# Optimization experiments

Hardware: AMD Instinct MI355X
Metric: run time of the kernel (lower is better)

The kernel has to match this reference:

```python
import jax, jax.numpy as jnp
import numpy as np

B, N, D = 2, 2048, 1024
H = 16
D_HEAD = D // H
WINDOW = 128


def setup_inputs() -> dict:
    key = jax.random.key(0)
    ks = jax.random.split(key, 9)
    s = 1.0 / np.sqrt(D)
    return {
        "x": jax.random.normal(ks[0], (B, N, D), dtype=jnp.float32),
        "Wq": jax.random.uniform(ks[1], (D, D), jnp.float32, -s, s),
        "bq": jax.random.uniform(ks[2], (D,), jnp.float32, -s, s),
        "Wk": jax.random.uniform(ks[3], (D, D), jnp.float32, -s, s),
        "bk": jax.random.uniform(ks[4], (D,), jnp.float32, -s, s),
        "Wv": jax.random.uniform(ks[5], (D, D), jnp.float32, -s, s),
        "bv": jax.random.uniform(ks[6], (D,), jnp.float32, -s, s),
        "Wo": jax.random.uniform(ks[7], (D, D), jnp.float32, -s, s),
        "bo": jax.random.uniform(ks[8], (D,), jnp.float32, -s, s),
    }


def reference(x, Wq, bq, Wk, bk, Wv, bv, Wo, bo):
    # Projections (torch Linear: x @ W.T + b), split into heads: (B,H,N,d)
    def proj(W, b):
        y = x @ W.T + b
        return y.reshape(B, N, H, D_HEAD).transpose(0, 2, 1, 3)

    Q = proj(Wq, bq)
    K = proj(Wk, bk)
    V = proj(Wv, bv)

    scale = 1.0 / np.sqrt(D_HEAD)
    scores = jnp.einsum("bhqd,bhkd->bhqk", Q, K) * scale  # (B,H,N,N)

    i = jnp.arange(N)[:, None]
    j = jnp.arange(N)[None, :]
    band = jnp.abs(i - j) <= WINDOW  # (N,N) sliding-window band mask
    scores = jnp.where(band, scores, -jnp.inf)

    probs = jax.nn.softmax(scores, axis=-1)
    out = jnp.einsum("bhqk,bhkd->bhqd", probs, V)  # (B,H,N,d)
    out = out.transpose(0, 2, 1, 3).reshape(B, N, D)
    return out @ Wo.T + bo
```

## Files before the change

kernel.cpp:

```cpp
#include <hip/hip_runtime.h>
#include <hip/hip_bf16.h>
#include <stdint.h>

typedef __bf16 bf16_t;
typedef __bf16 bf16x8 __attribute__((ext_vector_type(8)));
typedef float f32x4 __attribute__((ext_vector_type(4)));

#define NB 2
#define NN 2048
#define ND 1024
#define NH 16
#define DHEAD 64
#define WIN 128

__device__ __forceinline__ void load_lds16(const void* g, void* l) {
  __builtin_amdgcn_global_load_lds(
      (const __attribute__((address_space(1))) uint32_t*)g,
      (__attribute__((address_space(3))) uint32_t*)l, 16, 0, 0);
}

__global__ __launch_bounds__(256) void cast_kernel(const float* __restrict__ in,
                                                   bf16_t* __restrict__ out, int n4) {
  int i = blockIdx.x * 256 + threadIdx.x;
  if (i < n4) {
    float4 v = reinterpret_cast<const float4*>(in)[i];
    union { bf16_t h[4]; uint2 u; } o;
    o.h[0] = (bf16_t)v.x; o.h[1] = (bf16_t)v.y;
    o.h[2] = (bf16_t)v.z; o.h[3] = (bf16_t)v.w;
    reinterpret_cast<uint2*>(out)[i] = o.u;
  }
}

__global__ __launch_bounds__(256) void cast4_kernel(const float* __restrict__ i0, const float* __restrict__ i1,
                                                    const float* __restrict__ i2, const float* __restrict__ i3,
                                                    bf16_t* o0, bf16_t* o1, bf16_t* o2, bf16_t* o3, int n4) {
  int z = blockIdx.y;
  const float* in = (z == 0) ? i0 : (z == 1) ? i1 : (z == 2) ? i2 : i3;
  bf16_t* out = (z == 0) ? o0 : (z == 1) ? o1 : (z == 2) ? o2 : o3;
  int i = blockIdx.x * 256 + threadIdx.x;
  if (i < n4) {
    float4 v = reinterpret_cast<const float4*>(in)[i];
    union { bf16_t h[4]; uint2 u; } o;
    o.h[0] = (bf16_t)v.x; o.h[1] = (bf16_t)v.y;
    o.h[2] = (bf16_t)v.z; o.h[3] = (bf16_t)v.w;
    reinterpret_cast<uint2*>(out)[i] = o.u;
  }
}

__global__ __launch_bounds__(512, 4)
void qkv_gemm8(const bf16_t* __restrict__ xb,
               const bf16_t* __restrict__ Wqb, const bf16_t* __restrict__ Wkb,
               const bf16_t* __restrict__ Wvb,
               const float* __restrict__ bq, const float* __restrict__ bk,
               const float* __restrict__ bv,
               bf16_t* __restrict__ Qh, bf16_t* __restrict__ Kh,
               bf16_t* __restrict__ VTt) {
  __shared__ __align__(16) bf16_t lds[3][12288];

  const int raw = blockIdx.x;
  const int swz = (raw & 7) * 48 + (raw >> 3);
  const int mt = swz / 12, nt = swz % 12;
  const int m0 = mt * 128;
  const int z = nt >> 2;
  const int n0z = (nt & 3) * 256;
  const bf16_t* Bw  = (z == 0) ? Wqb : (z == 1) ? Wkb : Wvb;
  const float* bias = (z == 0) ? bq  : (z == 1) ? bk  : bv;

  const int tid = threadIdx.x, lane = tid & 63, w = tid >> 6;
  const int wm = w >> 2, wn = w & 3;
  const int lrow = lane & 15, lkg = lane >> 4;
  const int srow = lane >> 2;
  const int schunk = (lane & 3) ^ (srow & 3);

  const bf16_t* asrc  = xb + (size_t)(m0 + w * 16 + srow) * 1024 + schunk * 8;
  const bf16_t* bsrc0 = Bw + (size_t)(n0z + (w * 2) * 16 + srow) * 1024 + schunk * 8;
  const bf16_t* bsrc1 = bsrc0 + 16 * 1024;

  f32x4 acc[4][4] = {};

  auto stage = [&](int t) {
    const int tt = (t < 32) ? t : (t - 32);
    const int k0 = tt << 5;
    bf16_t* buf = &lds[t % 3][0];
    load_lds16(asrc + k0,  buf + w * 512);
    load_lds16(bsrc0 + k0, buf + 4096 + (w * 2) * 512);
    load_lds16(bsrc1 + k0, buf + 4096 + (w * 2 + 1) * 512);
  };

  stage(0);
  stage(1);
  asm volatile("s_waitcnt vmcnt(3)" ::: "memory");
  __builtin_amdgcn_s_barrier();

  for (int t = 0; t < 32; ++t) {
    const bf16_t* Abuf = &lds[t % 3][0];
    const bf16_t* Bbuf = Abuf + 4096;
    bf16x8 af[4], bf[4];
#pragma unroll
    for (int m = 0; m < 4; ++m) {
      const int row = wm * 64 + m * 16 + lrow;
      af[m] = *reinterpret_cast<const bf16x8*>(Abuf + row * 32 + ((lkg ^ (row & 3)) << 3));
    }
#pragma unroll
    for (int n = 0; n < 4; ++n) {
      const int row = wn * 64 + n * 16 + lrow;
      bf[n] = *reinterpret_cast<const bf16x8*>(Bbuf + row * 32 + ((lkg ^ (row & 3)) << 3));
    }
    stage(t + 2);
    __builtin_amdgcn_s_barrier();
    __builtin_amdgcn_s_setprio(1);
#pragma unroll
    for (int m = 0; m < 4; ++m)
#pragma unroll
      for (int n = 0; n < 4; ++n)
        acc[m][n] = __builtin_amdgcn_mfma_f32_16x16x32_bf16(af[m], bf[n], acc[m][n], 0, 0, 0);
    __builtin_amdgcn_s_setprio(0);
    asm volatile("s_waitcnt vmcnt(3)" ::: "memory");
    __builtin_amdgcn_s_barrier();
    __builtin_amdgcn_sched_barrier(0);
  }

#pragma unroll
  for (int m = 0; m < 4; ++m)
#pragma unroll
    for (int n = 0; n < 4; ++n)
#pragma unroll
      for (int r = 0; r < 4; ++r) {
        const int grow = m0 + wm * 64 + m * 16 + lkg * 4 + r;
        const int colz = n0z + wn * 64 + n * 16 + lrow;
        float val = acc[m][n][r] + bias[colz];
        const int bb = grow >> 11, tok = grow & 2047;
        const int hh = colz >> 6, dd = colz & 63;
        if (z == 2) {
          VTt[((((size_t)(bb * NH + hh) * 32 + (tok >> 6)) * 64 + dd) << 6) + (tok & 63)] = (bf16_t)val;
        } else {
          bf16_t* outp = (z == 0) ? Qh : Kh;
          outp[(((size_t)(bb * NH + hh) * NN + tok) << 6) + dd] = (bf16_t)val;
        }
      }
}

__device__ __forceinline__ void gemm_tile(const bf16_t* __restrict__ A,
                                          const bf16_t* __restrict__ Bw,
                                          bf16_t* As, bf16_t* Bs,
                                          int m0, int n0, f32x4 acc[4][4]) {
  const int tid  = threadIdx.x;
  const int lane = tid & 63;
  const int wid  = tid >> 6;
  const int wr = wid >> 1, wc = wid & 1;
  const int lrow = lane & 15, lkg = lane >> 4;
  const int srow = lane >> 2, scol = (lane & 3) * 8;

  for (int k0 = 0; k0 < 1024; k0 += 32) {
#pragma unroll
    for (int i = 0; i < 2; ++i) {
      const int rbase = (wid * 2 + i) * 16;
      load_lds16(A  + (size_t)(m0 + rbase + srow) * 1024 + k0 + scol, As + rbase * 32);
      load_lds16(Bw + (size_t)(n0 + rbase + srow) * 1024 + k0 + scol, Bs + rbase * 32);
    }
    __syncthreads();
    bf16x8 af[4], bf[4];
#pragma unroll
    for (int m = 0; m < 4; ++m)
      af[m] = *reinterpret_cast<const bf16x8*>(As + (wr * 64 + m * 16 + lrow) * 32 + lkg * 8);
#pragma unroll
    for (int n = 0; n < 4; ++n)
      bf[n] = *reinterpret_cast<const bf16x8*>(Bs + (wc * 64 + n * 16 + lrow) * 32 + lkg * 8);
#pragma unroll
    for (int m = 0; m < 4; ++m)
#pragma unroll
      for (int n = 0; n < 4; ++n)
        acc[m][n] = __builtin_amdgcn_mfma_f32_16x16x32_bf16(af[m], bf[n], acc[m][n], 0, 0, 0);
    __syncthreads();
  }
}

__global__ __launch_bounds__(256, 2)
void out_gemm(const bf16_t* __restrict__ AOb, const bf16_t* __restrict__ Wob,
              const float* __restrict__ bo, float* __restrict__ Cout) {
  __shared__ __align__(16) bf16_t As[128 * 32];
  __shared__ __align__(16) bf16_t Bs[128 * 32];
  const int m0 = blockIdx.y * 128, n0 = blockIdx.x * 128;
  f32x4 acc[4][4] = {};
  gemm_tile(AOb, Wob, As, Bs, m0, n0, acc);

  const int lane = threadIdx.x & 63;
  const int wid  = threadIdx.x >> 6;
  const int wr = wid >> 1, wc = wid & 1;
  const int lrow = lane & 15, lkg = lane >> 4;
#pragma unroll
  for (int m = 0; m < 4; ++m)
#pragma unroll
    for (int n = 0; n < 4; ++n)
#pragma unroll
      for (int r = 0; r < 4; ++r) {
        int row = m0 + wr * 64 + m * 16 + lkg * 4 + r;
        int col = n0 + wc * 64 + n * 16 + lrow;
        Cout[(size_t)row * 1024 + col] = acc[m][n][r] + bo[col];
      }
}

__global__ __launch_bounds__(256)
void attn_kernel(const bf16_t* __restrict__ Qh, const bf16_t* __restrict__ Kh,
                 const bf16_t* __restrict__ VTt, bf16_t* __restrict__ AO) {
  __shared__ __align__(16) bf16_t KV_lds[2][2][4096];
  __shared__ uint32_t P_lds[4][16][32];

  const int work = ((blockIdx.x & 7) << 7) | (blockIdx.x >> 3);
  const int qt = work & 31, h = (work >> 5) & 15, b = work >> 9;
  const int tid = threadIdx.x, lane = tid & 63, w = tid >> 6;
  const int lrow = lane & 15, lkg = lane >> 4;
  const int q0 = qt * 64;
  const int qb = q0 + w * 16;
  const int qrow = qb + lrow;
  const int rs7 = lrow & 7;

  const int srow8 = lane >> 3;
  const int sswz  = 8 * ((lane & 7) ^ srow8);

  const bf16_t* kbase = Kh  + ((size_t)(b * NH + h) * NN) * DHEAD;
  const bf16_t* vbase = VTt + ((size_t)(b * NH + h) * (NN / 64)) * DHEAD * 64;

  const bf16_t* qptr = Qh + (((size_t)(b * NH + h) * NN + qrow) << 6) + lkg * 8;
  bf16x8 qf0 = *reinterpret_cast<const bf16x8*>(qptr);
  bf16x8 qf1 = *reinterpret_cast<const bf16x8*>(qptr + 32);

  float m_run = -1e30f, l_run = 0.f;
  f32x4 o[4] = {};

  const int kstart = (q0 - WIN > 0) ? (q0 - WIN) : 0;
  const int kend = (q0 + 64 + WIN < NN) ? (q0 + 64 + WIN) : NN;
  const int nch = (kend - kstart) >> 6;
  const float scale = 0.125f;

  auto stage = [&](int bufi, int kc) {
#pragma unroll
    for (int j = 0; j < 2; ++j) {
      const int i = w * 2 + j;
      load_lds16(kbase + (((size_t)(kc + i * 8 + srow8)) << 6) + sswz,
                 &KV_lds[bufi][0][i * 512]);
      load_lds16(vbase + (((size_t)((kc >> 6) * 64 + i * 8 + srow8)) << 6) + sswz,
                 &KV_lds[bufi][1][i * 512]);
    }
  };

  stage(0, kstart);
  __syncthreads();

  for (int ic = 0; ic < nch; ++ic) {
    const int kc = kstart + ic * 64;
    const int bi = ic & 1;
    if (ic + 1 < nch) stage(bi ^ 1, kc + 64);

    const bf16_t* Kt = &KV_lds[bi][0][0];
    const bf16_t* Vt = &KV_lds[bi][1][0];

    f32x4 s[4];
#pragma unroll
    for (int t = 0; t < 4; ++t) {
      const bf16_t* kr = Kt + (t * 16 + lrow) * 64;
      bf16x8 kf0 = *reinterpret_cast<const bf16x8*>(kr + ((lkg ^ rs7) << 3));
      bf16x8 kf1 = *reinterpret_cast<const bf16x8*>(kr + (((4 + lkg) ^ rs7) << 3));
      f32x4 zz = {};
      zz = __builtin_amdgcn_mfma_f32_16x16x32_bf16(kf0, qf0, zz, 0, 0, 0);
      zz = __builtin_amdgcn_mfma_f32_16x16x32_bf16(kf1, qf1, zz, 0, 0, 0);
      s[t] = zz;
    }

    bf16x8 vf0[4], vf1[4];
#pragma unroll
    for (int f = 0; f < 4; ++f) {
      const bf16_t* vr = Vt + (f * 16 + lrow) * 64;
      vf0[f] = *reinterpret_cast<const bf16x8*>(vr + ((lkg ^ rs7) << 3));
      vf1[f] = *reinterpret_cast<const bf16x8*>(vr + (((4 + lkg) ^ rs7) << 3));
    }

    const bool needs_mask = (kc < qb - 113) || (kc > qb + 65);
    float p[4][4];
    float mloc = -1e30f, rsum = 0.f;
    if (needs_mask) {
      float v[4][4];
#pragma unroll
      for (int t = 0; t < 4; ++t)
#pragma unroll
        for (int r = 0; r < 4; ++r) {
          int k = kc + t * 16 + lkg * 4 + r;
          int d = qrow - k;
          bool ok = (unsigned)(d + WIN) <= 2u * WIN;
          v[t][r] = ok ? s[t][r] * scale : -1e30f;
          mloc = fmaxf(mloc, v[t][r]);
        }
      mloc = fmaxf(mloc, __shfl_xor(mloc, 16, 64));
      mloc = fmaxf(mloc, __shfl_xor(mloc, 32, 64));
      float mn = fmaxf(m_run, mloc);
      float corr = __expf(m_run - mn);
      m_run = mn;
#pragma unroll
      for (int t = 0; t < 4; ++t)
#pragma unroll
        for (int r = 0; r < 4; ++r) {
          int k = kc + t * 16 + lkg * 4 + r;
          int d = qrow - k;
          bool ok = (unsigned)(d + WIN) <= 2u * WIN;
          p[t][r] = ok ? __expf(v[t][r] - mn) : 0.f;
          rsum += p[t][r];
        }
      rsum += __shfl_xor(rsum, 16, 64);
      rsum += __shfl_xor(rsum, 32, 64);
      l_run = l_run * corr + rsum;
#pragma unroll
      for (int f = 0; f < 4; ++f) o[f] *= corr;
    } else {
      float v[4][4];
#pragma unroll
      for (int t = 0; t < 4; ++t)
#pragma unroll
        for (int r = 0; r < 4; ++r) {
          v[t][r] = s[t][r] * scale;
          mloc = fmaxf(mloc, v[t][r]);
        }
      mloc = fmaxf(mloc, __shfl_xor(mloc, 16, 64));
      mloc = fmaxf(mloc, __shfl_xor(mloc, 32, 64));
      float mn = fmaxf(m_run, mloc);
      float corr = __expf(m_run - mn);
      m_run = mn;
#pragma unroll
      for (int t = 0; t < 4; ++t)
#pragma unroll
        for (int r = 0; r < 4; ++r) {
          p[t][r] = __expf(v[t][r] - mn);
          rsum += p[t][r];
        }
      rsum += __shfl_xor(rsum, 16, 64);
      rsum += __shfl_xor(rsum, 32, 64);
      l_run = l_run * corr + rsum;
#pragma unroll
      for (int f = 0; f < 4; ++f) o[f] *= corr;
    }

    uint32_t* prow = &P_lds[w][lrow][0];
#pragma unroll
    for (int t = 0; t < 4; ++t)
#pragma unroll
      for (int c = 0; c < 2; ++c) {
        union { bf16_t hh[2]; uint32_t u; } pk;
        pk.hh[0] = (bf16_t)p[t][2 * c];
        pk.hh[1] = (bf16_t)p[t][2 * c + 1];
        int L = 8 * t + 2 * lkg + c;
        int pos = (((L >> 2) ^ rs7) << 2) | (L & 3);
        prow[pos] = pk.u;
      }
    asm volatile("" ::: "memory");
    const bf16_t* prd = reinterpret_cast<const bf16_t*>(&P_lds[w][lrow][0]);
    bf16x8 pa0 = *reinterpret_cast<const bf16x8*>(prd + ((lkg ^ rs7) << 3));
    bf16x8 pa1 = *reinterpret_cast<const bf16x8*>(prd + (((4 + lkg) ^ rs7) << 3));

#pragma unroll
    for (int f = 0; f < 4; ++f) {
      o[f] = __builtin_amdgcn_mfma_f32_16x16x32_bf16(vf0[f], pa0, o[f], 0, 0, 0);
      o[f] = __builtin_amdgcn_mfma_f32_16x16x32_bf16(vf1[f], pa1, o[f], 0, 0, 0);
    }
    __syncthreads();
  }

  float inv = 1.0f / l_run;
#pragma unroll
  for (int f = 0; f < 4; ++f) {
    union { bf16_t hh[4]; uint2 u; } ov;
#pragma unroll
    for (int r = 0; r < 4; ++r) ov.hh[r] = (bf16_t)(o[f][r] * inv);
    bf16_t* op = AO + (size_t)(b * NN + qrow) * ND + h * DHEAD + f * 16 + lkg * 4;
    *reinterpret_cast<uint2*>(op) = ov.u;
  }
}

extern "C" void kernel_launch(void* const* d_in, const int* in_sizes, int n_in,
                              void* d_out, int out_size, void* d_ws, size_t ws_size,
                              hipStream_t stream) {
  const float* x  = (const float*)d_in[0];
  const float* Wq = (const float*)d_in[1];
  const float* bq = (const float*)d_in[2];
  const float* Wk = (const float*)d_in[3];
  const float* bk = (const float*)d_in[4];
  const float* Wv = (const float*)d_in[5];
  const float* bv = (const float*)d_in[6];
  const float* Wo = (const float*)d_in[7];
  const float* bo = (const float*)d_in[8];
  float* out = (float*)d_out;

  bf16_t* ws  = (bf16_t*)d_ws;
  bf16_t* xb  = ws;
  bf16_t* Wqb = xb  + 4194304;
  bf16_t* Wkb = Wqb + 1048576;
  bf16_t* Wvb = Wkb + 1048576;
  bf16_t* Wob = Wvb + 1048576;
  bf16_t* Qh  = Wob + 1048576;
  bf16_t* Kh  = Qh  + 4194304;
  bf16_t* VTt = Kh  + 4194304;
  bf16_t* AOb = VTt + 4194304;

  cast_kernel<<<4096, 256, 0, stream>>>(x, xb, 1048576);
  cast4_kernel<<<dim3(1024, 4), 256, 0, stream>>>(Wq, Wk, Wv, Wo, Wqb, Wkb, Wvb, Wob, 262144);

  qkv_gemm8<<<384, 512, 0, stream>>>(xb, Wqb, Wkb, Wvb, bq, bk, bv, Qh, Kh, VTt);
  attn_kernel<<<1024, 256, 0, stream>>>(Qh, Kh, VTt, AOb);
  out_gemm<<<dim3(8, 32), 256, 0, stream>>>(AOb, Wob, bo, out);
}
```

Baseline: 103.9 us.

## Enlarge QKV GEMM tile to 256x256 with BK=64 double buffering

Changes the QKV projection GEMM from 128x256 tiles with a 3-stage BK=32 pipeline to 256x256 tiles with a 2-stage BK=64 pipeline, halving the grid to 192 blocks. Each wave now computes an 8x4 MFMA block, increasing arithmetic intensity and LDS reuse per global load while reducing the barrier count per K. It trades away occupancy (launch bounds 4 to 2, 128KB LDS per block) and leaves 192 blocks on a 256-CU device, so many CUs sit idle.

Result: slower. 117.2 us (+12.8%).

```diff
diff --git a/kernel.cpp b/kernel.cpp
--- a/kernel.cpp
+++ b/kernel.cpp
@@ -47,7 +47,7 @@
   }
 }
 
-__global__ __launch_bounds__(512, 4)
+__global__ __launch_bounds__(512, 2)
 void qkv_gemm8(const bf16_t* __restrict__ xb,
                const bf16_t* __restrict__ Wqb, const bf16_t* __restrict__ Wkb,
                const bf16_t* __restrict__ Wvb,
@@ -55,12 +55,12 @@
                const float* __restrict__ bv,
                bf16_t* __restrict__ Qh, bf16_t* __restrict__ Kh,
                bf16_t* __restrict__ VTt) {
-  __shared__ __align__(16) bf16_t lds[3][12288];
+  __shared__ __align__(16) bf16_t lds[2][32768];
 
   const int raw = blockIdx.x;
-  const int swz = (raw & 7) * 48 + (raw >> 3);
+  const int swz = (raw & 7) * 24 + (raw >> 3);
   const int mt = swz / 12, nt = swz % 12;
-  const int m0 = mt * 128;
+  const int m0 = mt * 256;
   const int z = nt >> 2;
   const int n0z = (nt & 3) * 256;
   const bf16_t* Bw  = (z == 0) ? Wqb : (z == 1) ? Wkb : Wvb;
@@ -69,64 +69,76 @@
   const int tid = threadIdx.x, lane = tid & 63, w = tid >> 6;
   const int wm = w >> 2, wn = w & 3;
   const int lrow = lane & 15, lkg = lane >> 4;
-  const int srow = lane >> 2;
-  const int schunk = (lane & 3) ^ (srow & 3);
-
-  const bf16_t* asrc  = xb + (size_t)(m0 + w * 16 + srow) * 1024 + schunk * 8;
-  const bf16_t* bsrc0 = Bw + (size_t)(n0z + (w * 2) * 16 + srow) * 1024 + schunk * 8;
-  const bf16_t* bsrc1 = bsrc0 + 16 * 1024;
-
-  f32x4 acc[4][4] = {};
-
-  auto stage = [&](int t) {
-    const int tt = (t < 32) ? t : (t - 32);
-    const int k0 = tt << 5;
-    bf16_t* buf = &lds[t % 3][0];
-    load_lds16(asrc + k0,  buf + w * 512);
-    load_lds16(bsrc0 + k0, buf + 4096 + (w * 2) * 512);
-    load_lds16(bsrc1 + k0, buf + 4096 + (w * 2 + 1) * 512);
+
+  const int sr  = lane >> 3;
+  const int sc  = ((lane & 7) ^ sr) * 8;
+  const bf16_t* asrc = xb + (size_t)(m0 + w * 32 + sr) * 1024 + sc;
+  const bf16_t* bsrc = Bw + (size_t)(n0z + w * 32 + sr) * 1024 + sc;
+
+  f32x4 acc[8][4] = {};
+
+  auto stage = [&](int buf, int t) {
+    const int k0 = t << 6;
+    bf16_t* adst = &lds[buf][w * 2048];
+    bf16_t* bdst = &lds[buf][16384 + w * 2048];
+#pragma unroll
+    for (int j = 0; j < 4; ++j) {
+      load_lds16(asrc + (size_t)j * 8192 + k0, adst + j * 512);
+      load_lds16(bsrc + (size_t)j * 8192 + k0, bdst + j * 512);
+    }
   };
 
-  stage(0);
-  stage(1);
-  asm volatile("s_waitcnt vmcnt(3)" ::: "memory");
+  stage(0, 0);
+  asm volatile("s_waitcnt vmcnt(0)" ::: "memory");
   __builtin_amdgcn_s_barrier();
-
-  for (int t = 0; t < 32; ++t) {
-    const bf16_t* Abuf = &lds[t % 3][0];
-    const bf16_t* Bbuf = Abuf + 4096;
-    bf16x8 af[4], bf[4];
-#pragma unroll
-    for (int m = 0; m < 4; ++m) {
-      const int row = wm * 64 + m * 16 + lrow;
-      af[m] = *reinterpret_cast<const bf16x8*>(Abuf + row * 32 + ((lkg ^ (row & 3)) << 3));
-    }
-#pragma unroll
-    for (int n = 0; n < 4; ++n) {
-      const int row = wn * 64 + n * 16 + lrow;
-      bf[n] = *reinterpret_cast<const bf16x8*>(Bbuf + row * 32 + ((lkg ^ (row & 3)) << 3));
-    }
-    stage(t + 2);
+  asm volatile("" ::: "memory");
+
+  for (int t = 0; t < 16; ++t) {
+    const int cur = t & 1;
+    if (t < 15) {
+      stage(cur ^ 1, t + 1);
+      asm volatile("s_waitcnt vmcnt(8)" ::: "memory");
+    } else {
+      asm volatile("s_waitcnt vmcnt(0)" ::: "memory");
+    }
     __builtin_amdgcn_s_barrier();
-    __builtin_amdgcn_s_setprio(1);
-#pragma unroll
-    for (int m = 0; m < 4; ++m)
-#pragma unroll
-      for (int n = 0; n < 4; ++n)
-        acc[m][n] = __builtin_amdgcn_mfma_f32_16x16x32_bf16(af[m], bf[n], acc[m][n], 0, 0, 0);
-    __builtin_amdgcn_s_setprio(0);
-    asm volatile("s_waitcnt vmcnt(3)" ::: "memory");
+    asm volatile("" ::: "memory");
+
+    const bf16_t* Abuf = &lds[cur][0];
+    const bf16_t* Bbuf = &lds[cur][16384];
+#pragma unroll
+    for (int s = 0; s < 2; ++s) {
+      bf16x8 af[8], bf[4];
+#pragma unroll
+      for (int m = 0; m < 8; ++m) {
+        const int row = wm * 128 + m * 16 + lrow;
+        af[m] = *reinterpret_cast<const bf16x8*>(Abuf + row * 64 + (((s * 4 + lkg) ^ (row & 7)) << 3));
+      }
+#pragma unroll
+      for (int n = 0; n < 4; ++n) {
+        const int row = wn * 64 + n * 16 + lrow;
+        bf[n] = *reinterpret_cast<const bf16x8*>(Bbuf + row * 64 + (((s * 4 + lkg) ^ (row & 7)) << 3));
+      }
+      __builtin_amdgcn_s_setprio(1);
+#pragma unroll
+      for (int m = 0; m < 8; ++m)
+#pragma unroll
+        for (int n = 0; n < 4; ++n)
+          acc[m][n] = __builtin_amdgcn_mfma_f32_16x16x32_bf16(af[m], bf[n], acc[m][n], 0, 0, 0);
+      __builtin_amdgcn_s_setprio(0);
+    }
+    asm volatile("" ::: "memory");
     __builtin_amdgcn_s_barrier();
-    __builtin_amdgcn_sched_barrier(0);
-  }
-
-#pragma unroll
-  for (int m = 0; m < 4; ++m)
+    asm volatile("" ::: "memory");
+  }
+
+#pragma unroll
+  for (int m = 0; m < 8; ++m)
 #pragma unroll
     for (int n = 0; n < 4; ++n)
 #pragma unroll
       for (int r = 0; r < 4; ++r) {
-        const int grow = m0 + wm * 64 + m * 16 + lkg * 4 + r;
+        const int grow = m0 + wm * 128 + m * 16 + lkg * 4 + r;
         const int colz = n0z + wn * 64 + n * 16 + lrow;
         float val = acc[m][n][r] + bias[colz];
         const int bb = grow >> 11, tok = grow & 2047;
@@ -402,7 +414,7 @@
   cast_kernel<<<4096, 256, 0, stream>>>(x, xb, 1048576);
   cast4_kernel<<<dim3(1024, 4), 256, 0, stream>>>(Wq, Wk, Wv, Wo, Wqb, Wkb, Wvb, Wob, 262144);
 
-  qkv_gemm8<<<384, 512, 0, stream>>>(xb, Wqb, Wkb, Wvb, bq, bk, bv, Qh, Kh, VTt);
+  qkv_gemm8<<<192, 512, 0, stream>>>(xb, Wqb, Wkb, Wvb, bq, bk, bv, Qh, Kh, VTt);
   attn_kernel<<<1024, 256, 0, stream>>>(Qh, Kh, VTt, AOb);
   out_gemm<<<dim3(8, 32), 256, 0, stream>>>(AOb, Wob, bo, out);
 }
```
